# Kernel optimization log

Hardware: AMD Instinct MI355X
Metric: run time of the kernel (lower is better)

The kernel has to match this reference:

```python
import jax, jax.numpy as jnp
import numpy as np

HEADS = 16
DIM_HEAD = 64


def setup_inputs() -> dict:
    key = jax.random.key(0)
    k1, k2, k3 = jax.random.split(key, 3)
    b, n, dim = 8, 4096, 1024
    inner = HEADS * DIM_HEAD  # 1024
    x = jax.random.normal(k1, (b, n, dim), dtype=jnp.float32)
    # torch Linear stored transposed; here W_qkv is [in, out] so y = x @ W_qkv
    W_qkv = jax.random.normal(k2, (dim, 4 * inner), dtype=jnp.float32) * (dim ** -0.5)
    W_out = jax.random.normal(k3, (inner, dim), dtype=jnp.float32) * (inner ** -0.5)
    b_out = jnp.zeros((dim,), dtype=jnp.float32)
    return {"x": x, "W_qkv": W_qkv, "W_out": W_out, "b_out": b_out}


def reference(x, W_qkv, W_out, b_out):
    b, n, dim = x.shape
    h, d = HEADS, DIM_HEAD
    scale = d ** -0.5
    qkv = x @ W_qkv  # [b, n, 4*h*d]
    q, k, v, v2 = jnp.split(qkv, 4, axis=-1)
    # rearrange 'b n (h d) -> b h n d'
    to_heads = lambda t: t.reshape(b, n, h, d).transpose(0, 2, 1, 3)
    q, k, v, v2 = map(to_heads, (q, k, v, v2))
    # channel-wise attention: dots = q^T @ k over the sequence axis -> [b,h,d,d]
    dots = jnp.einsum('bhnd,bhne->bhde', q, k) * scale
    attn = jax.nn.softmax(dots, axis=-1)
    # v^T @ v2 -> [b,h,d,d]
    vv = jnp.einsum('bhnd,bhne->bhde', v, v2)
    out = jnp.einsum('bhde,bhef->bhdf', attn, vv)  # [b,h,d,d]
    # rearrange 'b h n d -> b n (h d)' with n == dim_head here
    out = out.transpose(0, 2, 1, 3).reshape(b, d, h * d)  # [b, dim_head, inner]
    return out @ W_out + b_out  # [b, dim_head, dim]
```

## Files before the change

### kernel.cpp

```cpp
#include <hip/hip_runtime.h>
#include <hip/hip_bf16.h>
#include <stdint.h>

typedef _Float16 f16;
typedef _Float16 f16x8 __attribute__((ext_vector_type(8)));
typedef float f32x4 __attribute__((ext_vector_type(4)));

#define AS1 __attribute__((address_space(1)))
#define AS3 __attribute__((address_space(3)))

__global__ __launch_bounds__(256) void tr_cvt_kernel(
    const float* __restrict__ src, f16* __restrict__ dst, int R, int C)
{
    __shared__ float tile[64][65];
    const int b = blockIdx.z;
    src += (size_t)b * R * C;
    dst += (size_t)b * R * C;
    const int c0 = blockIdx.x * 64;
    const int r0 = blockIdx.y * 64;
    const int t = threadIdx.x;
    {
        const int cc = (t & 15) * 4;
        const int rr = t >> 4;
#pragma unroll
        for (int p = 0; p < 4; ++p) {
            const int r = rr + p * 16;
            const float4 v = *(const float4*)(src + (size_t)(r0 + r) * C + c0 + cc);
            tile[r][cc + 0] = v.x; tile[r][cc + 1] = v.y;
            tile[r][cc + 2] = v.z; tile[r][cc + 3] = v.w;
        }
    }
    __syncthreads();
    {
        const int rq = (t & 15) * 4;
        const int cp = t >> 4;
#pragma unroll
        for (int p = 0; p < 4; ++p) {
            const int c = cp + p * 16;
            ushort4 o;
            f16 h0 = (f16)tile[rq + 0][c];
            f16 h1 = (f16)tile[rq + 1][c];
            f16 h2 = (f16)tile[rq + 2][c];
            f16 h3 = (f16)tile[rq + 3][c];
            o.x = __builtin_bit_cast(unsigned short, h0);
            o.y = __builtin_bit_cast(unsigned short, h1);
            o.z = __builtin_bit_cast(unsigned short, h2);
            o.w = __builtin_bit_cast(unsigned short, h3);
            *(ushort4*)(dst + (size_t)(c0 + c) * R + r0 + rq) = o;
        }
    }
}

__device__ __forceinline__ void stage256(
    const f16* __restrict__ src, int ld, char* ldsbase, int tid)
{
    const int lane = tid & 63;
    const int gch = ((lane & 7) ^ (lane >> 3)) * 8;
    const int rowl = tid >> 3;
    const int wbase = (tid >> 3) & ~7;
#pragma unroll
    for (int p = 0; p < 4; ++p) {
        const f16* s = src + (size_t)(p * 64 + rowl) * ld + gch;
        __builtin_amdgcn_global_load_lds(
            (const AS1 uint32_t*)s,
            (AS3 uint32_t*)(ldsbase + (p * 64 + wbase) * 128), 16, 0, 0);
    }
}

__device__ __forceinline__ void gemm256_core(
    const f16* __restrict__ A, const f16* __restrict__ Bt,
    int lda, int ldb, int nsteps,
    f16* As, f16* Bs, f32x4 (&acc)[8][4], int tid)
{
    const int lane = tid & 63, w = tid >> 6;
    const int wr = w >> 2, wc = w & 3;
    const int cl = lane & 15, kg = lane >> 4, b7 = lane & 7;

    stage256(A, lda, (char*)As, tid);
    stage256(Bt, ldb, (char*)Bs, tid);

    for (int t = 0; t < nsteps; ++t) {
        const int cur = t & 1;
        if (t + 1 < nsteps) {
            const int k0 = (t + 1) * 64;
            stage256(A + k0, lda, (char*)As + (cur ^ 1) * 32768, tid);
            stage256(Bt + k0, ldb, (char*)Bs + (cur ^ 1) * 32768, tid);
            asm volatile("s_waitcnt vmcnt(8)" ::: "memory");
        } else {
            asm volatile("s_waitcnt vmcnt(0)" ::: "memory");
        }
        __builtin_amdgcn_s_barrier();
        const f16* Ab = As + cur * 16384;
        const f16* Bb = Bs + cur * 16384;
#pragma unroll
        for (int kk = 0; kk < 2; ++kk) {
            const int ch = (kk * 4 + kg) ^ b7;
            f16x8 af[8], bf[4];
#pragma unroll
            for (int i = 0; i < 8; ++i)
                af[i] = *(const f16x8*)&Ab[(wr * 128 + i * 16 + cl) * 64 + ch * 8];
#pragma unroll
            for (int j = 0; j < 4; ++j)
                bf[j] = *(const f16x8*)&Bb[(wc * 64 + j * 16 + cl) * 64 + ch * 8];
#pragma unroll
            for (int i = 0; i < 8; ++i)
#pragma unroll
                for (int j = 0; j < 4; ++j)
                    acc[i][j] = __builtin_amdgcn_mfma_f32_16x16x32_f16(af[i], bf[j], acc[i][j], 0, 0, 0);
        }
        __builtin_amdgcn_s_barrier();
    }
}

__global__ __launch_bounds__(512) void gemm_syk256(
    const f16* __restrict__ xT, f16* __restrict__ Gp)
{
    __shared__ f16 As[2 * 256 * 64];
    __shared__ f16 Bs[2 * 256 * 64];
    const int orig = blockIdx.x;
    const int l = (orig & 7) * 32 + (orig >> 3);
    const int tile = l & 15, b = (l >> 4) & 7, s = l >> 7;
    const int ti = tile >> 2, tj = tile & 3;

    const f16* base = xT + (size_t)b * (1024 * 4096) + (size_t)s * 2048;
    const f16* A  = base + (size_t)ti * 256 * 4096;
    const f16* Bt = base + (size_t)tj * 256 * 4096;

    f32x4 acc[8][4];
#pragma unroll
    for (int i = 0; i < 8; ++i)
#pragma unroll
        for (int j = 0; j < 4; ++j) acc[i][j] = f32x4{0.f, 0.f, 0.f, 0.f};

    gemm256_core(A, Bt, 4096, 4096, 32, As, Bs, acc, threadIdx.x);

    f16* out = Gp + ((size_t)s * 8 + b) * 1048576;
    const int lane = threadIdx.x & 63, w = threadIdx.x >> 6;
    const int wr = w >> 2, wc = w & 3;
    const int cl = lane & 15, rg = lane >> 4;
#pragma unroll
    for (int i = 0; i < 8; ++i)
#pragma unroll
        for (int j = 0; j < 4; ++j)
#pragma unroll
            for (int q = 0; q < 4; ++q) {
                const int row = ti * 256 + wr * 128 + i * 16 + rg * 4 + q;
                const int col = tj * 256 + wc * 64 + j * 16 + cl;
                out[(size_t)row * 1024 + col] = (f16)acc[i][j][q];
            }
}

__global__ __launch_bounds__(256) void reduce_sum(
    const f16* __restrict__ Gp, f16* __restrict__ G)
{
    const size_t i = ((size_t)blockIdx.x * 256 + threadIdx.x) * 8;
    const f16x8 a = *(const f16x8*)(Gp + i);
    const f16x8 c = *(const f16x8*)(Gp + 8388608 + i);
    f16x8 o;
#pragma unroll
    for (int j = 0; j < 8; ++j) o[j] = (f16)((float)a[j] + (float)c[j]);
    *(f16x8*)(G + i) = o;
}

__global__ __launch_bounds__(512) void gemm_qv256(
    const f16* __restrict__ WqkvT, const f16* __restrict__ G,
    f16* __restrict__ UW2)
{
    __shared__ f16 As[2 * 256 * 64];
    __shared__ f16 Bs[2 * 256 * 64];
    const int orig = blockIdx.x;
    const int l = (orig & 7) * 32 + (orig >> 3);
    const int bx = l & 3, by = (l >> 2) & 7, b = l >> 5;
    const int arow = (by < 4) ? by * 256 : 2048 + (by - 4) * 256;

    const f16* A  = WqkvT + (size_t)arow * 1024;
    const f16* Bt = G + (size_t)b * 1048576 + (size_t)bx * 256 * 1024;

    f32x4 acc[8][4];
#pragma unroll
    for (int i = 0; i < 8; ++i)
#pragma unroll
        for (int j = 0; j < 4; ++j) acc[i][j] = f32x4{0.f, 0.f, 0.f, 0.f};

    gemm256_core(A, Bt, 1024, 1024, 16, As, Bs, acc, threadIdx.x);

    f16* C = UW2 + (size_t)b * 2097152;
    const int lane = threadIdx.x & 63, w = threadIdx.x >> 6;
    const int wr = w >> 2, wc = w & 3;
    const int cl = lane & 15, rg = lane >> 4;
#pragma unroll
    for (int i = 0; i < 8; ++i)
#pragma unroll
        for (int j = 0; j < 4; ++j) {
            const int cc = bx * 256 + wc * 64 + j * 16 + cl;
#pragma unroll
            for (int q = 0; q < 4; ++q) {
                const int rr = by * 256 + wr * 128 + i * 16 + rg * 4 + q;
                C[(size_t)rr * 1024 + cc] = (f16)acc[i][j][q];
            }
        }
}

__device__ __forceinline__ void gemm_body(
    const f16* __restrict__ A, const f16* __restrict__ Bt,
    int lda, int ldb, int K, f16* As, f16* Bs,
    f32x4 (&acc)[4][4], int tid)
{
    const int lane = tid & 63, w = tid >> 6;
    const int wr = w >> 1, wc = w & 1;
    const int lrow = lane >> 3;
    const int lcol = (lane & 7) * 8;
    for (int k0 = 0; k0 < K; k0 += 64) {
#pragma unroll
        for (int p = 0; p < 4; ++p) {
            const f16* sa = A + (size_t)(p * 32 + w * 8 + lrow) * lda + k0 + lcol;
            __builtin_amdgcn_global_load_lds(
                (const AS1 uint32_t*)sa,
                (AS3 uint32_t*)((char*)As + p * 4096 + w * 1024), 16, 0, 0);
            const f16* sb = Bt + (size_t)(p * 32 + w * 8 + lrow) * ldb + k0 + lcol;
            __builtin_amdgcn_global_load_lds(
                (const AS1 uint32_t*)sb,
                (AS3 uint32_t*)((char*)Bs + p * 4096 + w * 1024), 16, 0, 0);
        }
        __syncthreads();
#pragma unroll
        for (int kk = 0; kk < 2; ++kk) {
            f16x8 af[4], bfr[4];
#pragma unroll
            for (int i = 0; i < 4; ++i)
                af[i] = *(const f16x8*)&As[(wr * 64 + i * 16 + (lane & 15)) * 64 + kk * 32 + (lane >> 4) * 8];
#pragma unroll
            for (int j = 0; j < 4; ++j)
                bfr[j] = *(const f16x8*)&Bs[(wc * 64 + j * 16 + (lane & 15)) * 64 + kk * 32 + (lane >> 4) * 8];
#pragma unroll
            for (int i = 0; i < 4; ++i)
#pragma unroll
                for (int j = 0; j < 4; ++j)
                    acc[i][j] = __builtin_amdgcn_mfma_f32_16x16x32_f16(af[i], bfr[j], acc[i][j], 0, 0, 0);
        }
        __syncthreads();
    }
}

__global__ __launch_bounds__(256) void bias_init(
    const float* __restrict__ bias, float* __restrict__ out)
{
    const int idx = blockIdx.x * 1024 + threadIdx.x * 4;
    const float4 bv = *(const float4*)(bias + (idx & 1023));
    *(float4*)(out + idx) = bv;
}

__global__ __launch_bounds__(256) void gemm_out(
    const f16* __restrict__ A, const f16* __restrict__ Bt,
    float* __restrict__ Cout)
{
    __shared__ f16 As[128 * 64];
    __shared__ f16 Bs[128 * 64];
    const int tn0 = blockIdx.x * 128;
    const int tm0 = blockIdx.y * 128;
    const int s = blockIdx.z;
    f32x4 acc[4][4];
#pragma unroll
    for (int i = 0; i < 4; ++i)
#pragma unroll
        for (int j = 0; j < 4; ++j) acc[i][j] = f32x4{0.f, 0.f, 0.f, 0.f};

    gemm_body(A + (size_t)tm0 * 1024 + s * 512,
              Bt + (size_t)tn0 * 1024 + s * 512, 1024, 1024, 512,
              As, Bs, acc, threadIdx.x);

    const int lane = threadIdx.x & 63, w = threadIdx.x >> 6;
    const int wr = w >> 1, wc = w & 1;
    const int cl = lane & 15, rg = lane >> 4;
#pragma unroll
    for (int i = 0; i < 4; ++i)
#pragma unroll
        for (int j = 0; j < 4; ++j) {
            const int cc = tn0 + wc * 64 + j * 16 + cl;
#pragma unroll
            for (int q = 0; q < 4; ++q) {
                const int rr = tm0 + wr * 64 + i * 16 + rg * 4 + q;
                atomicAdd(&Cout[(size_t)rr * 1024 + cc], acc[i][j][q]);
            }
        }
}

__global__ __launch_bounds__(512) void attn_small(
    const f16* __restrict__ UW2, const f16* __restrict__ WqkvT,
    f16* __restrict__ O)
{
    __shared__ float dots[64][66];
    __shared__ float vv[64][66];
    const int h = blockIdx.x, b = blockIdx.y;
    const int tid = threadIdx.x, lane = tid & 63, w = tid >> 6;
    const int isVV = w >> 2;
    const int kq = w & 3;

    const f16* Arows = UW2 + (size_t)b * (2048 * 1024)
                           + (size_t)isVV * (1024 * 1024) + (size_t)h * 64 * 1024;
    const f16* Brows = WqkvT + (size_t)(isVV ? 3072 : 1024) * 1024 + (size_t)h * 64 * 1024;

    f32x4 acc[4][4];
#pragma unroll
    for (int i = 0; i < 4; ++i)
#pragma unroll
        for (int j = 0; j < 4; ++j) acc[i][j] = f32x4{0.f, 0.f, 0.f, 0.f};

    const int cl = lane & 15, kg = lane >> 4;
    for (int ks = 0; ks < 8; ++ks) {
        const int k0 = kq * 256 + ks * 32 + kg * 8;
        f16x8 af[4], bfr[4];
#pragma unroll
        for (int i = 0; i < 4; ++i)
            af[i] = *(const f16x8*)(Arows + (size_t)(i * 16 + cl) * 1024 + k0);
#pragma unroll
        for (int j = 0; j < 4; ++j)
            bfr[j] = *(const f16x8*)(Brows + (size_t)(j * 16 + cl) * 1024 + k0);
#pragma unroll
        for (int i = 0; i < 4; ++i)
#pragma unroll
            for (int j = 0; j < 4; ++j)
                acc[i][j] = __builtin_amdgcn_mfma_f32_16x16x32_f16(af[i], bfr[j], acc[i][j], 0, 0, 0);
    }

    float (*dst)[66] = isVV ? vv : dots;
#pragma unroll
    for (int r = 0; r < 4; ++r) {
        if (kq == r) {
            if (r == 0) {
#pragma unroll
                for (int i = 0; i < 4; ++i)
#pragma unroll
                    for (int j = 0; j < 4; ++j)
#pragma unroll
                        for (int q = 0; q < 4; ++q)
                            dst[i * 16 + kg * 4 + q][j * 16 + cl] = acc[i][j][q];
            } else {
#pragma unroll
                for (int i = 0; i < 4; ++i)
#pragma unroll
                    for (int j = 0; j < 4; ++j)
#pragma unroll
                        for (int q = 0; q < 4; ++q)
                            dst[i * 16 + kg * 4 + q][j * 16 + cl] += acc[i][j][q];
            }
        }
        __syncthreads();
    }

    if (tid < 64) {
        const int r = tid;
        float mx = -1e30f;
        for (int e = 0; e < 64; ++e) {
            const float v = dots[r][e] * 0.125f;
            dots[r][e] = v;
            mx = fmaxf(mx, v);
        }
        float s = 0.f;
        for (int e = 0; e < 64; ++e) {
            const float v = __expf(dots[r][e] - mx);
            dots[r][e] = v;
            s += v;
        }
        const float inv = 1.f / s;
        for (int e = 0; e < 64; ++e) dots[r][e] *= inv;
    }
    __syncthreads();

    {
        const int r = tid >> 3, f0 = (tid & 7) * 8;
        float o[8];
#pragma unroll
        for (int i = 0; i < 8; ++i) o[i] = 0.f;
        for (int e = 0; e < 64; ++e) {
            const float a = dots[r][e];
#pragma unroll
            for (int i = 0; i < 8; ++i) o[i] += a * vv[e][f0 + i];
        }
        f16* Od = O + (size_t)b * 64 * 1024 + (size_t)r * 1024 + h * 64 + f0;
#pragma unroll
        for (int i = 0; i < 8; ++i) Od[i] = (f16)o[i];
    }
}

extern "C" void kernel_launch(void* const* d_in, const int* in_sizes, int n_in,
                              void* d_out, int out_size, void* d_ws, size_t ws_size,
                              hipStream_t stream)
{
    const float* x    = (const float*)d_in[0];
    const float* Wqkv = (const float*)d_in[1];
    const float* Wout = (const float*)d_in[2];
    const float* bout = (const float*)d_in[3];

    char* ws = (char*)d_ws;
    f16* xT    = (f16*)(ws + 0);
    f16* WqkvT = (f16*)(ws + 67108864);
    f16* WoutT = (f16*)(ws + 75497472);
    f16* G     = (f16*)(ws + 77594624);
    f16* Gp    = (f16*)(ws + 94371840);
    f16* UW2   = (f16*)(ws + 94371840);
    f16* O     = (f16*)(ws + 127926272);

    tr_cvt_kernel<<<dim3(16, 64, 8), 256, 0, stream>>>(x, xT, 4096, 1024);
    tr_cvt_kernel<<<dim3(64, 16, 1), 256, 0, stream>>>(Wqkv, WqkvT, 1024, 4096);
    tr_cvt_kernel<<<dim3(16, 16, 1), 256, 0, stream>>>(Wout, WoutT, 1024, 1024);

    gemm_syk256<<<256, 512, 0, stream>>>(xT, Gp);
    reduce_sum<<<4096, 256, 0, stream>>>(Gp, G);
    gemm_qv256<<<256, 512, 0, stream>>>(WqkvT, G, UW2);
    attn_small<<<dim3(16, 8), 512, 0, stream>>>(UW2, WqkvT, O);
    bias_init<<<512, 256, 0, stream>>>(bout, (float*)d_out);
    gemm_out<<<dim3(8, 4, 2), 256, 0, stream>>>(O, WoutT, (float*)d_out);
}
```

Baseline: 194.2 us.

## Restructure 256x256 GEMM core into 4-stage K=32 pipeline with split staging

Replaces the double-buffered K=64 GEMM mainloop with a four-slot ring of K=32 tiles prefetched three steps ahead. Loads for A and B are issued at different points inside each step, interleaved with two half-MFMA blocks, and s_setprio is raised around the MFMA sections. LDS per block stays at 128 KB and launch bounds now request 2 blocks per CU. The aim is to hide global-load latency and LDS waits better, at the cost of more barriers per unit of K and a more complex swizzle.

```diff
diff --git a/kernel.cpp b/kernel.cpp
--- a/kernel.cpp
+++ b/kernel.cpp
@@ -51,72 +51,100 @@
     }
 }
 
-__device__ __forceinline__ void stage256(
-    const f16* __restrict__ src, int ld, char* ldsbase, int tid)
-{
-    const int lane = tid & 63;
-    const int gch = ((lane & 7) ^ (lane >> 3)) * 8;
-    const int rowl = tid >> 3;
-    const int wbase = (tid >> 3) & ~7;
-#pragma unroll
-    for (int p = 0; p < 4; ++p) {
-        const f16* s = src + (size_t)(p * 64 + rowl) * ld + gch;
-        __builtin_amdgcn_global_load_lds(
-            (const AS1 uint32_t*)s,
-            (AS3 uint32_t*)(ldsbase + (p * 64 + wbase) * 128), 16, 0, 0);
-    }
-}
-
-__device__ __forceinline__ void gemm256_core(
-    const f16* __restrict__ A, const f16* __restrict__ Bt,
-    int lda, int ldb, int nsteps,
-    f16* As, f16* Bs, f32x4 (&acc)[8][4], int tid)
+__device__ __forceinline__ void stage32(
+    const f16* __restrict__ src, int ld, f16* lds_slot, int tid)
+{
+    const int r0 = tid >> 2;
+    const int cd = tid & 3;
+#pragma unroll
+    for (int p = 0; p < 2; ++p) {
+        const int R = p * 128 + r0;
+        const int gch = cd ^ ((R >> 1) & 3);
+        const f16* s = src + (size_t)R * ld + gch * 8;
+        f16* d = lds_slot + (p * 128 + ((tid >> 6) << 4)) * 32;
+        __builtin_amdgcn_global_load_lds((const AS1 uint32_t*)s,
+                                         (AS3 uint32_t*)d, 16, 0, 0);
+    }
+}
+
+template <int VM, bool STAGE>
+__device__ __forceinline__ void tile_step(
+    const f16* __restrict__ Ag, int lda,
+    const f16* __restrict__ Bg, int ldb,
+    f16* stA, f16* stB,
+    const f16* cA, const f16* cB,
+    int aoff, int boff,
+    f32x4 (&acc)[8][4], int tid)
+{
+    asm volatile("s_waitcnt vmcnt(%0)" :: "n"(VM) : "memory");
+    if (STAGE) stage32(Ag, lda, stA, tid);
+    __builtin_amdgcn_s_barrier();
+    f16x8 af[4], bf[4];
+#pragma unroll
+    for (int i = 0; i < 4; ++i) af[i] = *(const f16x8*)&cA[aoff + i * 512];
+#pragma unroll
+    for (int j = 0; j < 4; ++j) bf[j] = *(const f16x8*)&cB[boff + j * 512];
+    __builtin_amdgcn_s_setprio(1);
+#pragma unroll
+    for (int i = 0; i < 4; ++i)
+#pragma unroll
+        for (int j = 0; j < 4; ++j)
+            acc[i][j] = __builtin_amdgcn_mfma_f32_16x16x32_f16(af[i], bf[j], acc[i][j], 0, 0, 0);
+    __builtin_amdgcn_s_setprio(0);
+    __builtin_amdgcn_s_barrier();
+    if (STAGE) stage32(Bg, ldb, stB, tid);
+#pragma unroll
+    for (int i = 0; i < 4; ++i) af[i] = *(const f16x8*)&cA[aoff + 2048 + i * 512];
+    __builtin_amdgcn_s_setprio(1);
+#pragma unroll
+    for (int i = 0; i < 4; ++i)
+#pragma unroll
+        for (int j = 0; j < 4; ++j)
+            acc[i + 4][j] = __builtin_amdgcn_mfma_f32_16x16x32_f16(af[i], bf[j], acc[i + 4][j], 0, 0, 0);
+    __builtin_amdgcn_s_setprio(0);
+    __builtin_amdgcn_s_barrier();
+}
+
+template <int T>
+__device__ __forceinline__ void gemm256_v2(
+    const f16* __restrict__ A, int lda,
+    const f16* __restrict__ Bt, int ldb,
+    f16 (*AsS)[256 * 32], f16 (*BsS)[256 * 32],
+    f32x4 (&acc)[8][4], int tid)
 {
     const int lane = tid & 63, w = tid >> 6;
     const int wr = w >> 2, wc = w & 3;
-    const int cl = lane & 15, kg = lane >> 4, b7 = lane & 7;
-
-    stage256(A, lda, (char*)As, tid);
-    stage256(Bt, ldb, (char*)Bs, tid);
-
-    for (int t = 0; t < nsteps; ++t) {
-        const int cur = t & 1;
-        if (t + 1 < nsteps) {
-            const int k0 = (t + 1) * 64;
-            stage256(A + k0, lda, (char*)As + (cur ^ 1) * 32768, tid);
-            stage256(Bt + k0, ldb, (char*)Bs + (cur ^ 1) * 32768, tid);
-            asm volatile("s_waitcnt vmcnt(8)" ::: "memory");
-        } else {
-            asm volatile("s_waitcnt vmcnt(0)" ::: "memory");
-        }
-        __builtin_amdgcn_s_barrier();
-        const f16* Ab = As + cur * 16384;
-        const f16* Bb = Bs + cur * 16384;
-#pragma unroll
-        for (int kk = 0; kk < 2; ++kk) {
-            const int ch = (kk * 4 + kg) ^ b7;
-            f16x8 af[8], bf[4];
-#pragma unroll
-            for (int i = 0; i < 8; ++i)
-                af[i] = *(const f16x8*)&Ab[(wr * 128 + i * 16 + cl) * 64 + ch * 8];
-#pragma unroll
-            for (int j = 0; j < 4; ++j)
-                bf[j] = *(const f16x8*)&Bb[(wc * 64 + j * 16 + cl) * 64 + ch * 8];
-#pragma unroll
-            for (int i = 0; i < 8; ++i)
-#pragma unroll
-                for (int j = 0; j < 4; ++j)
-                    acc[i][j] = __builtin_amdgcn_mfma_f32_16x16x32_f16(af[i], bf[j], acc[i][j], 0, 0, 0);
-        }
-        __builtin_amdgcn_s_barrier();
-    }
-}
-
-__global__ __launch_bounds__(512) void gemm_syk256(
+    const int cl = lane & 15, kg = lane >> 4;
+    const int ch = kg ^ ((cl >> 1) & 3);
+    const int aoff = (wr * 128 + cl) * 32 + ch * 8;
+    const int boff = (wc * 64 + cl) * 32 + ch * 8;
+
+#pragma unroll
+    for (int t = 0; t < 3; ++t) {
+        stage32(A + t * 32, lda, AsS[t], tid);
+        stage32(Bt + t * 32, ldb, BsS[t], tid);
+    }
+#pragma unroll 1
+    for (int t = 0; t < T - 3; ++t) {
+        const int cs = t & 3, ss = (t + 3) & 3;
+        tile_step<8, true>(A + (size_t)(t + 3) * 32, lda,
+                           Bt + (size_t)(t + 3) * 32, ldb,
+                           AsS[ss], BsS[ss], AsS[cs], BsS[cs],
+                           aoff, boff, acc, tid);
+    }
+    tile_step<8, false>(A, lda, Bt, ldb, AsS[0], BsS[0],
+                        AsS[(T - 3) & 3], BsS[(T - 3) & 3], aoff, boff, acc, tid);
+    tile_step<4, false>(A, lda, Bt, ldb, AsS[0], BsS[0],
+                        AsS[(T - 2) & 3], BsS[(T - 2) & 3], aoff, boff, acc, tid);
+    tile_step<0, false>(A, lda, Bt, ldb, AsS[0], BsS[0],
+                        AsS[(T - 1) & 3], BsS[(T - 1) & 3], aoff, boff, acc, tid);
+}
+
+__global__ __launch_bounds__(512, 2) void gemm_syk256(
     const f16* __restrict__ xT, f16* __restrict__ Gp)
 {
-    __shared__ f16 As[2 * 256 * 64];
-    __shared__ f16 Bs[2 * 256 * 64];
+    __shared__ f16 AsS[4][256 * 32];
+    __shared__ f16 BsS[4][256 * 32];
     const int orig = blockIdx.x;
     const int l = (orig & 7) * 32 + (orig >> 3);
     const int tile = l & 15, b = (l >> 4) & 7, s = l >> 7;
@@ -132,7 +160,7 @@
 #pragma unroll
         for (int j = 0; j < 4; ++j) acc[i][j] = f32x4{0.f, 0.f, 0.f, 0.f};
 
-    gemm256_core(A, Bt, 4096, 4096, 32, As, Bs, acc, threadIdx.x);
+    gemm256_v2<64>(A, 4096, Bt, 4096, AsS, BsS, acc, threadIdx.x);
 
     f16* out = Gp + ((size_t)s * 8 + b) * 1048576;
     const int lane = threadIdx.x & 63, w = threadIdx.x >> 6;
@@ -162,12 +190,12 @@
     *(f16x8*)(G + i) = o;
 }
 
-__global__ __launch_bounds__(512) void gemm_qv256(
+__global__ __launch_bounds__(512, 2) void gemm_qv256(
     const f16* __restrict__ WqkvT, const f16* __restrict__ G,
     f16* __restrict__ UW2)
 {
-    __shared__ f16 As[2 * 256 * 64];
-    __shared__ f16 Bs[2 * 256 * 64];
+    __shared__ f16 AsS[4][256 * 32];
+    __shared__ f16 BsS[4][256 * 32];
     const int orig = blockIdx.x;
     const int l = (orig & 7) * 32 + (orig >> 3);
     const int bx = l & 3, by = (l >> 2) & 7, b = l >> 5;
@@ -182,7 +210,7 @@
 #pragma unroll
         for (int j = 0; j < 4; ++j) acc[i][j] = f32x4{0.f, 0.f, 0.f, 0.f};
 
-    gemm256_core(A, Bt, 1024, 1024, 16, As, Bs, acc, threadIdx.x);
+    gemm256_v2<32>(A, 1024, Bt, 1024, AsS, BsS, acc, threadIdx.x);
 
     f16* C = UW2 + (size_t)b * 2097152;
     const int lane = threadIdx.x & 63, w = threadIdx.x >> 6;
```

Result: slower. 206.8 us (+6.5%).
